# Performance work log

Measured on AMD Instinct MI355X. Metric: run time of the kernel, lower is better.

Reference implementation:

```python
import jax, jax.numpy as jnp
import numpy as np

N_NODES = 100_000
N_EDGES = 1_600_000
D_IN, D_HID, D_OUT = 256, 64, 32
NUM_PROP = 10
ALPHA = 0.1


def setup_inputs() -> dict:
    key = jax.random.key(0)
    ks = jax.random.split(key, 8)
    features = jax.random.normal(ks[0], (N_NODES, D_IN), dtype=jnp.float32)
    row = jax.random.randint(ks[1], (N_EDGES,), 0, N_NODES, dtype=jnp.int32)
    col = jax.random.randint(ks[2], (N_EDGES,), 0, N_NODES, dtype=jnp.int32)
    # positive edge weights (stand-in for symmetric-normalized adjacency values)
    edge_vals = jax.random.uniform(ks[3], (N_EDGES,), dtype=jnp.float32) / 16.0
    W1 = jax.random.normal(ks[4], (D_IN, D_HID), dtype=jnp.float32) / np.sqrt(D_IN)
    b1 = jnp.zeros((D_HID,), dtype=jnp.float32)
    W2 = jax.random.normal(ks[5], (D_HID, D_OUT), dtype=jnp.float32) / np.sqrt(D_HID)
    b2 = jnp.zeros((D_OUT,), dtype=jnp.float32)
    return {"features": features, "row": row, "col": col, "edge_vals": edge_vals,
            "W1": W1, "b1": b1, "W2": W2, "b2": b2}


def _spmm(row, col, vals, x):
    # COO sparse-dense matmul: out[r] += vals[e] * x[col[e]] for each edge e
    return jax.ops.segment_sum(vals[:, None] * x[col], row, num_segments=N_NODES)


def reference(features, row, col, edge_vals, W1, b1, W2, b2):
    # head_transform: 2-layer MLP
    x = jax.nn.relu(features @ W1 + b1) @ W2 + b2  # [N, D_OUT]
    x0 = x
    # APPNP propagation: x = (1-alpha) * (A @ x) + alpha * x0
    def body(_, x):
        return (1.0 - ALPHA) * _spmm(row, col, edge_vals, x) + ALPHA * x0
    x = jax.lax.fori_loop(0, NUM_PROP, body, x)
    return x
```

## Files before the change

kernel.cpp:

```cpp
#include <hip/hip_runtime.h>

#define N_NODES 100000
#define N_EDGES 1600000
#define D_IN    256
#define D_HID   64
#define D_OUT   32
#define NPROP   10

#define NBUCK 196
#define CHUNK 6080
#define NCHUNK ((N_EDGES + CHUNK - 1) / CHUNK)

typedef _Float16 half_t;
typedef _Float16 h8  __attribute__((ext_vector_type(8)));
typedef _Float16 h4  __attribute__((ext_vector_type(4)));
typedef float    f4v __attribute__((ext_vector_type(4)));

__global__ __launch_bounds__(256) void pack_kernel(
    const float* __restrict__ W1, const float* __restrict__ W2,
    half_t* __restrict__ W1T, half_t* __restrict__ W2T)
{
  int t = blockIdx.x * 256 + threadIdx.x;
  if (t < 64 * 256) { int n = t >> 8, k = t & 255; W1T[t] = (half_t)W1[k * 64 + n]; }
  if (t < 32 * 64)  { int n = t >> 6, k = t & 63;  W2T[t] = (half_t)W2[k * 32 + n]; }
}

#define HSTRIDE 72

__global__ __launch_bounds__(256) void mlp_kernel(
    const float* __restrict__ F, const half_t* __restrict__ W1T,
    const float* __restrict__ b1, const half_t* __restrict__ W2T,
    const float* __restrict__ b2, half_t* __restrict__ x0h)
{
  __shared__ half_t h_lds[16 * HSTRIDE];
  __shared__ half_t out_lds[16 * 32];
  int t = threadIdx.x;
  int w = t >> 6, lane = t & 63;
  int m = lane & 15, q = lane >> 4;
  int node0 = blockIdx.x * 16;
  int hid0 = w * 16;

  f4v acc = {0.f, 0.f, 0.f, 0.f};
  const float* arow = F + (size_t)(node0 + m) * D_IN + q * 8;
  const half_t* brow = W1T + (size_t)(hid0 + m) * D_IN + q * 8;
#pragma unroll
  for (int s = 0; s < 8; ++s) {
    float4 f0 = *(const float4*)(arow + s * 32);
    float4 f1 = *(const float4*)(arow + s * 32 + 4);
    h8 a;
    a[0] = (_Float16)f0.x; a[1] = (_Float16)f0.y;
    a[2] = (_Float16)f0.z; a[3] = (_Float16)f0.w;
    a[4] = (_Float16)f1.x; a[5] = (_Float16)f1.y;
    a[6] = (_Float16)f1.z; a[7] = (_Float16)f1.w;
    h8 b = *(const h8*)(brow + s * 32);
    acc = __builtin_amdgcn_mfma_f32_16x16x32_f16(a, b, acc, 0, 0, 0);
  }

  {
    int col = hid0 + m;
    float bb = b1[col];
#pragma unroll
    for (int i = 0; i < 4; ++i) {
      float hv = fmaxf(acc[i] + bb, 0.f);
      h_lds[(q * 4 + i) * HSTRIDE + col] = (half_t)hv;
    }
  }
  __syncthreads();

  if (w < 2) {
    f4v acc2 = {0.f, 0.f, 0.f, 0.f};
    int out0 = w * 16;
#pragma unroll
    for (int s = 0; s < 2; ++s) {
      h8 a = *(const h8*)(h_lds + m * HSTRIDE + s * 32 + q * 8);
      h8 b = *(const h8*)(W2T + (size_t)(out0 + m) * D_HID + s * 32 + q * 8);
      acc2 = __builtin_amdgcn_mfma_f32_16x16x32_f16(a, b, acc2, 0, 0, 0);
    }
    int oc = out0 + m;
    float b2v = b2[oc];
#pragma unroll
    for (int i = 0; i < 4; ++i)
      out_lds[(q * 4 + i) * 32 + oc] = (half_t)(acc2[i] + b2v);
  }
  __syncthreads();

  if (t < 64) {
    int nl = t >> 2, qq = t & 3;
    *(int4*)(x0h + (size_t)(node0 + nl) * D_OUT + qq * 8) =
        *(const int4*)(out_lds + nl * 32 + qq * 8);
  }
}

__global__ __launch_bounds__(256) void bhist_kernel(
    const int* __restrict__ row, int* __restrict__ bcnt)
{
  __shared__ int lb[NBUCK];
  int t = threadIdx.x;
  for (int i = t; i < NBUCK; i += 256) lb[i] = 0;
  __syncthreads();
  int stride = gridDim.x * 256;
  for (int e = blockIdx.x * 256 + t; e < N_EDGES; e += stride)
    atomicAdd(&lb[row[e] >> 9], 1);
  __syncthreads();
  for (int i = t; i < NBUCK; i += 256)
    if (lb[i]) atomicAdd(&bcnt[i], lb[i]);
}

__global__ __launch_bounds__(256) void bscan_kernel(
    const int* __restrict__ bcnt, int* __restrict__ bbase, int* __restrict__ pbase)
{
  __shared__ int l1[256], l2[256];
  int t = threadIdx.x;
  int a = (t < NBUCK) ? bcnt[t] : 0;
  int r = (t < NBUCK) ? (((a + 3) & ~3) + 3 * 512) : 0;
  l1[t] = a; l2[t] = r;
  __syncthreads();
  for (int off = 1; off < 256; off <<= 1) {
    int x1 = (t >= off) ? l1[t - off] : 0;
    int x2 = (t >= off) ? l2[t - off] : 0;
    __syncthreads();
    l1[t] += x1; l2[t] += x2;
    __syncthreads();
  }
  if (t < NBUCK) { bbase[t] = l1[t] - a; pbase[t] = l2[t] - r; }
  if (t == NBUCK - 1) { bbase[NBUCK] = l1[t]; pbase[NBUCK] = l2[t]; }
}

__global__ __launch_bounds__(256) void bscatter_kernel(
    const int* __restrict__ row, const int* __restrict__ col,
    const float* __restrict__ vals, int* __restrict__ bfill,
    const int* __restrict__ bbase, int2* __restrict__ ebuck)
{
  __shared__ int2 img[CHUNK];
  __shared__ unsigned short sbk[CHUNK];
  __shared__ int cnt[NBUCK], base[NBUCK], gb[NBUCK], fil[NBUCK];
  __shared__ int ssc[256];
  int t = threadIdx.x;
  int e0 = blockIdx.x * CHUNK;
  int n = min(CHUNK, N_EDGES - e0);

  for (int i = t; i < NBUCK; i += 256) { cnt[i] = 0; fil[i] = 0; }
  __syncthreads();
  for (int i = t; i < n; i += 256) atomicAdd(&cnt[row[e0 + i] >> 9], 1);
  __syncthreads();
  int c = (t < NBUCK) ? cnt[t] : 0;
  ssc[t] = c;
  __syncthreads();
  for (int off = 1; off < 256; off <<= 1) {
    int add = (t >= off) ? ssc[t - off] : 0;
    __syncthreads();
    ssc[t] += add;
    __syncthreads();
  }
  if (t < NBUCK) {
    base[t] = ssc[t] - c;
    gb[t] = c ? atomicAdd(&bfill[t], c) : 0;
  }
  __syncthreads();
  for (int i = t; i < n; i += 256) {
    int r = row[e0 + i];
    int bk = r >> 9;
    int p = base[bk] + atomicAdd(&fil[bk], 1);
    img[p] = make_int2(col[e0 + i] | ((r & 511) << 17),
                       __float_as_int(vals[e0 + i]));
    sbk[p] = (unsigned short)bk;
  }
  __syncthreads();
  for (int i = t; i < n; i += 256) {
    int bk = sbk[i];
    ebuck[bbase[bk] + gb[bk] + (i - base[bk])] = img[i];
  }
}

__global__ __launch_bounds__(256) void bsort_kernel(
    const int* __restrict__ bbase, const int* __restrict__ pbase,
    const int2* __restrict__ ebuck, int2* __restrict__ epack,
    int* __restrict__ row_ptr)
{
  __shared__ int acnt[512], loff[513], lfill[512], ssc[256];
  int b = blockIdx.x, t = threadIdx.x;
  int r0 = b * 512;
  int nr = min(512, N_NODES - r0);
  int eb = bbase[b];
  int ne = bbase[b + 1] - eb;
  int pb = pbase[b];

  acnt[t] = 0; acnt[t + 256] = 0;
  lfill[t] = 0; lfill[t + 256] = 0;
  __syncthreads();
  for (int i = t; i < ne; i += 256)
    atomicAdd(&acnt[((unsigned)ebuck[eb + i].x) >> 17], 1);
  __syncthreads();
  int i0 = 2 * t, i1 = 2 * t + 1;
  int a0 = acnt[i0], a1 = acnt[i1];
  int p0 = (a0 + 3) & ~3, p1 = (a1 + 3) & ~3;
  int s = p0 + p1;
  ssc[t] = s;
  __syncthreads();
  for (int off = 1; off < 256; off <<= 1) {
    int add = (t >= off) ? ssc[t - off] : 0;
    __syncthreads();
    ssc[t] += add;
    __syncthreads();
  }
  int ex = ssc[t] - s;
  loff[i0] = ex;
  loff[i1] = ex + p0;
  if (t == 255) loff[512] = ssc[255];
  __syncthreads();
  int T = ssc[255];
  int slack = (pbase[b + 1] - pb) - T;
  int units = min(slack >> 2, nr);
  if (i0 < nr) row_ptr[r0 + i0] = pb + loff[i0] + 4 * min(i0, units);
  if (i1 < nr) row_ptr[r0 + i1] = pb + loff[i1] + 4 * min(i1, units);
  if (b == NBUCK - 1 && t == 0)
    row_ptr[N_NODES] = pb + loff[nr] + 4 * units;
  __syncthreads();
  for (int i = t; i < ne; i += 256) {
    int2 ed = ebuck[eb + i];
    int lr = ((unsigned)ed.x) >> 17;
    int cl = ed.x & 0x1FFFF;
    int p = loff[lr] + 4 * min(lr, units) + atomicAdd(&lfill[lr], 1);
    epack[pb + p] = make_int2(cl, ed.y);
  }
  __syncthreads();
  for (int i = t; i < nr; i += 256) {
    int a = acnt[i];
    int size_i = ((a + 3) & ~3) + 4 * (i < units);
    int st = loff[i] + 4 * min(i, units);
    for (int p = st + a; p < st + size_i; ++p)
      epack[pb + p] = make_int2(0, 0);
  }
}

__global__ __launch_bounds__(256) void spmm_kernel(
    const int* __restrict__ rp, const int2* __restrict__ ep,
    const half_t* __restrict__ xin, const half_t* __restrict__ x0h,
    half_t* __restrict__ xout, float* __restrict__ fout, int last)
{
  int gt = blockIdx.x * 256 + threadIdx.x;
  int r = gt >> 3;
  int c4 = (gt & 7) * 4;
  if (r >= N_NODES) return;
  int e0 = rp[r], e1 = rp[r + 1];

  float acc[4] = {0.f, 0.f, 0.f, 0.f};
  for (int e = e0; e < e1; e += 4) {
    int2 p0 = ep[e];
    int2 p1 = ep[e + 1];
    int2 p2 = ep[e + 2];
    int2 p3 = ep[e + 3];
    h4 g0 = *(const h4*)(xin + (size_t)p0.x * D_OUT + c4);
    h4 g1 = *(const h4*)(xin + (size_t)p1.x * D_OUT + c4);
    h4 g2 = *(const h4*)(xin + (size_t)p2.x * D_OUT + c4);
    h4 g3 = *(const h4*)(xin + (size_t)p3.x * D_OUT + c4);
    float v0 = __int_as_float(p0.y);
    float v1 = __int_as_float(p1.y);
    float v2 = __int_as_float(p2.y);
    float v3 = __int_as_float(p3.y);
#pragma unroll
    for (int j = 0; j < 4; ++j) {
      acc[j] = fmaf(v0, (float)g0[j], acc[j]);
      acc[j] = fmaf(v1, (float)g1[j], acc[j]);
      acc[j] = fmaf(v2, (float)g2[j], acc[j]);
      acc[j] = fmaf(v3, (float)g3[j], acc[j]);
    }
  }

  h4 x0v = *(const h4*)(x0h + (size_t)r * D_OUT + c4);
  if (last) {
    float4 o;
    o.x = 0.9f * acc[0] + 0.1f * (float)x0v[0];
    o.y = 0.9f * acc[1] + 0.1f * (float)x0v[1];
    o.z = 0.9f * acc[2] + 0.1f * (float)x0v[2];
    o.w = 0.9f * acc[3] + 0.1f * (float)x0v[3];
    *(float4*)(fout + (size_t)r * D_OUT + c4) = o;
  } else {
    h4 o;
#pragma unroll
    for (int j = 0; j < 4; ++j)
      o[j] = (half_t)(0.9f * acc[j] + 0.1f * (float)x0v[j]);
    *(h4*)(xout + (size_t)r * D_OUT + c4) = o;
  }
}

extern "C" void kernel_launch(void* const* d_in, const int* in_sizes, int n_in,
                              void* d_out, int out_size, void* d_ws, size_t ws_size,
                              hipStream_t stream) {
  const float* F     = (const float*)d_in[0];
  const int*   row   = (const int*)  d_in[1];
  const int*   col   = (const int*)  d_in[2];
  const float* evals = (const float*)d_in[3];
  const float* W1    = (const float*)d_in[4];
  const float* b1    = (const float*)d_in[5];
  const float* W2    = (const float*)d_in[6];
  const float* b2    = (const float*)d_in[7];
  float* out = (float*)d_out;

  char* w = (char*)d_ws;
  half_t* x0h    = (half_t*)(w);
  half_t* P      = (half_t*)(w +  6400000);
  half_t* Q      = (half_t*)(w + 12800000);
  int2*   ebuck  = (int2*)  (w +  6400000);
  int2*   epack  = (int2*)  (w + 19200000);
  int*   row_ptr = (int*)   (w + 34600192);
  int*   bcnt    = (int*)   (w + 35000576);
  int*   bfill   = (int*)   (w + 35001600);
  int*   bbase   = (int*)   (w + 35002624);
  int*   pbase   = (int*)   (w + 35003648);
  half_t* W1T    = (half_t*)(w + 35004672);
  half_t* W2T    = (half_t*)(w + 35037440);

  pack_kernel<<<64, 256, 0, stream>>>(W1, W2, W1T, W2T);
  mlp_kernel<<<N_NODES / 16, 256, 0, stream>>>(F, W1T, b1, W2T, b2, x0h);

  hipMemsetAsync(bcnt, 0, 2048, stream);
  bhist_kernel<<<640, 256, 0, stream>>>(row, bcnt);
  bscan_kernel<<<1, 256, 0, stream>>>(bcnt, bbase, pbase);
  bscatter_kernel<<<NCHUNK, 256, 0, stream>>>(row, col, evals, bfill, bbase, ebuck);
  bsort_kernel<<<NBUCK, 256, 0, stream>>>(bbase, pbase, ebuck, epack, row_ptr);

  const int grid_spmm = (N_NODES * 8 + 255) / 256;
  for (int i = 0; i < NPROP; ++i) {
    const half_t* xin = (i == 0) ? x0h : ((i & 1) ? P : Q);
    half_t* xout = (i & 1) ? Q : P;
    int last = (i == NPROP - 1);
    spmm_kernel<<<grid_spmm, 256, 0, stream>>>(
        row_ptr, epack, xin, x0h, xout, out, last);
  }
}
```

Baseline: 554.9 us.

## Restructure MLP kernel so each wave computes a full 16-node tile

The MLP kernel now gives each wave its own 16-node tile and all 64 hidden columns, instead of splitting the hidden columns of one tile across four waves. Each feature row is read from global memory by only one wave rather than four, which cuts redundant fp32 feature loads. The second layer now runs on every wave. The grid shrinks by four and the last tile index is clamped, so the final partial block recomputes and rewrites the same last nodes. The change raises register pressure (four accumulators) and adds a launch-bounds occupancy hint.

```diff
diff --git a/kernel.cpp b/kernel.cpp
--- a/kernel.cpp
+++ b/kernel.cpp
@@ -27,67 +27,90 @@
 
 #define HSTRIDE 72
 
-__global__ __launch_bounds__(256) void mlp_kernel(
+__global__ __launch_bounds__(256, 4) void mlp_kernel(
     const float* __restrict__ F, const half_t* __restrict__ W1T,
     const float* __restrict__ b1, const half_t* __restrict__ W2T,
     const float* __restrict__ b2, half_t* __restrict__ x0h)
 {
-  __shared__ half_t h_lds[16 * HSTRIDE];
-  __shared__ half_t out_lds[16 * 32];
+  __shared__ half_t h_lds[4 * 16 * HSTRIDE];
+  __shared__ half_t out_lds[4 * 16 * 32];
   int t = threadIdx.x;
   int w = t >> 6, lane = t & 63;
   int m = lane & 15, q = lane >> 4;
-  int node0 = blockIdx.x * 16;
-  int hid0 = w * 16;
-
-  f4v acc = {0.f, 0.f, 0.f, 0.f};
-  const float* arow = F + (size_t)(node0 + m) * D_IN + q * 8;
-  const half_t* brow = W1T + (size_t)(hid0 + m) * D_IN + q * 8;
-#pragma unroll
-  for (int s = 0; s < 8; ++s) {
-    float4 f0 = *(const float4*)(arow + s * 32);
-    float4 f1 = *(const float4*)(arow + s * 32 + 4);
-    h8 a;
-    a[0] = (_Float16)f0.x; a[1] = (_Float16)f0.y;
-    a[2] = (_Float16)f0.z; a[3] = (_Float16)f0.w;
-    a[4] = (_Float16)f1.x; a[5] = (_Float16)f1.y;
-    a[6] = (_Float16)f1.z; a[7] = (_Float16)f1.w;
-    h8 b = *(const h8*)(brow + s * 32);
-    acc = __builtin_amdgcn_mfma_f32_16x16x32_f16(a, b, acc, 0, 0, 0);
-  }
-
+  int gw = blockIdx.x * 4 + w;
+  int node0 = gw * 16;
+  if (node0 > N_NODES - 16) node0 = N_NODES - 16;
+
+  f4v acc[4];
+#pragma unroll
+  for (int i = 0; i < 4; ++i) acc[i] = (f4v){0.f, 0.f, 0.f, 0.f};
+
+  const float* ap = F + (size_t)(node0 + m) * D_IN + q * 8;
+
+#pragma unroll
+  for (int h = 0; h < 2; ++h) {
+    h8 af[4];
+#pragma unroll
+    for (int s = 0; s < 4; ++s) {
+      float4 f0 = *(const float4*)(ap + h * 128 + s * 32);
+      float4 f1 = *(const float4*)(ap + h * 128 + s * 32 + 4);
+      h8 a;
+      a[0] = (_Float16)f0.x; a[1] = (_Float16)f0.y;
+      a[2] = (_Float16)f0.z; a[3] = (_Float16)f0.w;
+      a[4] = (_Float16)f1.x; a[5] = (_Float16)f1.y;
+      a[6] = (_Float16)f1.z; a[7] = (_Float16)f1.w;
+      af[s] = a;
+    }
+    const half_t* bp = W1T + (size_t)m * D_IN + h * 128 + q * 8;
+#pragma unroll
+    for (int s = 0; s < 4; ++s) {
+      h8 b0 = *(const h8*)(bp + 0 * 16 * D_IN + s * 32);
+      h8 b1v = *(const h8*)(bp + 1 * 16 * D_IN + s * 32);
+      h8 b2v = *(const h8*)(bp + 2 * 16 * D_IN + s * 32);
+      h8 b3v = *(const h8*)(bp + 3 * 16 * D_IN + s * 32);
+      acc[0] = __builtin_amdgcn_mfma_f32_16x16x32_f16(af[s], b0, acc[0], 0, 0, 0);
+      acc[1] = __builtin_amdgcn_mfma_f32_16x16x32_f16(af[s], b1v, acc[1], 0, 0, 0);
+      acc[2] = __builtin_amdgcn_mfma_f32_16x16x32_f16(af[s], b2v, acc[2], 0, 0, 0);
+      acc[3] = __builtin_amdgcn_mfma_f32_16x16x32_f16(af[s], b3v, acc[3], 0, 0, 0);
+    }
+  }
+
+  half_t* hw = h_lds + w * 16 * HSTRIDE;
+#pragma unroll
+  for (int ht = 0; ht < 4; ++ht) {
+    float bb = b1[ht * 16 + m];
+#pragma unroll
+    for (int i = 0; i < 4; ++i) {
+      float hv = fmaxf(acc[ht][i] + bb, 0.f);
+      hw[(q * 4 + i) * HSTRIDE + ht * 16 + m] = (half_t)hv;
+    }
+  }
+  __syncthreads();
+
+  f4v o0 = {0.f, 0.f, 0.f, 0.f}, o1 = {0.f, 0.f, 0.f, 0.f};
+#pragma unroll
+  for (int s = 0; s < 2; ++s) {
+    h8 a = *(const h8*)(hw + m * HSTRIDE + s * 32 + q * 8);
+    h8 bb0 = *(const h8*)(W2T + (size_t)m * D_HID + s * 32 + q * 8);
+    h8 bb1 = *(const h8*)(W2T + (size_t)(16 + m) * D_HID + s * 32 + q * 8);
+    o0 = __builtin_amdgcn_mfma_f32_16x16x32_f16(a, bb0, o0, 0, 0, 0);
+    o1 = __builtin_amdgcn_mfma_f32_16x16x32_f16(a, bb1, o1, 0, 0, 0);
+  }
+  half_t* ow = out_lds + w * 16 * 32;
   {
-    int col = hid0 + m;
-    float bb = b1[col];
+    float c0 = b2[m], c1 = b2[16 + m];
 #pragma unroll
     for (int i = 0; i < 4; ++i) {
-      float hv = fmaxf(acc[i] + bb, 0.f);
-      h_lds[(q * 4 + i) * HSTRIDE + col] = (half_t)hv;
-    }
-  }
-  __syncthreads();
-
-  if (w < 2) {
-    f4v acc2 = {0.f, 0.f, 0.f, 0.f};
-    int out0 = w * 16;
-#pragma unroll
-    for (int s = 0; s < 2; ++s) {
-      h8 a = *(const h8*)(h_lds + m * HSTRIDE + s * 32 + q * 8);
-      h8 b = *(const h8*)(W2T + (size_t)(out0 + m) * D_HID + s * 32 + q * 8);
-      acc2 = __builtin_amdgcn_mfma_f32_16x16x32_f16(a, b, acc2, 0, 0, 0);
-    }
-    int oc = out0 + m;
-    float b2v = b2[oc];
-#pragma unroll
-    for (int i = 0; i < 4; ++i)
-      out_lds[(q * 4 + i) * 32 + oc] = (half_t)(acc2[i] + b2v);
-  }
-  __syncthreads();
-
-  if (t < 64) {
-    int nl = t >> 2, qq = t & 3;
+      ow[(q * 4 + i) * 32 + m]      = (half_t)(o0[i] + c0);
+      ow[(q * 4 + i) * 32 + 16 + m] = (half_t)(o1[i] + c1);
+    }
+  }
+  __syncthreads();
+
+  {
+    int nl = lane >> 2, qq = lane & 3;
     *(int4*)(x0h + (size_t)(node0 + nl) * D_OUT + qq * 8) =
-        *(const int4*)(out_lds + nl * 32 + qq * 8);
+        *(const int4*)(ow + nl * 32 + qq * 8);
   }
 }
 
@@ -312,7 +335,7 @@
   half_t* W2T    = (half_t*)(w + 35037440);
 
   pack_kernel<<<64, 256, 0, stream>>>(W1, W2, W1T, W2T);
-  mlp_kernel<<<N_NODES / 16, 256, 0, stream>>>(F, W1T, b1, W2T, b2, x0h);
+  mlp_kernel<<<(N_NODES / 16 + 3) / 4, 256, 0, stream>>>(F, W1T, b1, W2T, b2, x0h);
 
   hipMemsetAsync(bcnt, 0, 2048, stream);
   bhist_kernel<<<640, 256, 0, stream>>>(row, bcnt);
```

Result: faster. 532.1 us (-4.1%).
